# Kernel tuning notes

Hardware: AMD Instinct MI355X
Metric: run time of the kernel (lower is better)

Reference implementation:

```python
import jax, jax.numpy as jnp
import numpy as np
import math

D_MODEL = 1024
NUM_HEADS = 16
D_HEAD = D_MODEL // NUM_HEADS
BATCH = 2
SEQ = 2048


def setup_inputs() -> dict:
    key = jax.random.key(0)
    ks = jax.random.split(key, 5)
    sigma = math.sqrt(2.0 / (D_MODEL + D_MODEL))
    x = jax.random.normal(ks[0], (BATCH, SEQ, D_MODEL), dtype=jnp.float32)
    WQ = jax.random.normal(ks[1], (D_MODEL, D_MODEL), dtype=jnp.float32) * sigma
    WK = jax.random.normal(ks[2], (D_MODEL, D_MODEL), dtype=jnp.float32) * sigma
    WV = jax.random.normal(ks[3], (D_MODEL, D_MODEL), dtype=jnp.float32) * sigma
    WO = jax.random.normal(ks[4], (D_MODEL, D_MODEL), dtype=jnp.float32) * sigma
    return {"x": x, "WQ": WQ, "WK": WK, "WV": WV, "WO": WO}


def _softmax_fp32(scores):
    # matches custom softmax: compute in fp32, cast back to input dtype
    dtype = scores.dtype
    s = scores.astype(jnp.float32)
    return jax.nn.softmax(s, axis=-1).astype(dtype)


def reference(x, WQ, WK, WV, WO):
    batch, seq_len, _ = x.shape
    def split_heads(t):
        return t.reshape(batch, seq_len, NUM_HEADS, D_HEAD).transpose(0, 2, 1, 3)
    Q = split_heads(x @ WQ.T)  # [b,h,s,d]
    K = split_heads(x @ WK.T)
    V = split_heads(x @ WV.T)
    scale = 1.0 / math.sqrt(D_HEAD)
    scores = jnp.einsum('bhqd,bhkd->bhqk', Q, K) * scale
    # precomputed additive causal mask: 0 on/below diag, -inf above
    causal = jnp.triu(jnp.full((seq_len, seq_len), -jnp.inf, dtype=scores.dtype), k=1)
    scores = scores + causal
    attn = _softmax_fp32(scores)
    out = jnp.einsum('bhqk,bhkd->bhqd', attn, V)  # [b,h,s,d]
    out = out.transpose(0, 2, 1, 3).reshape(batch, seq_len, D_MODEL)
    return out @ WO.T
```

## Files before the change

### kernel.cpp

```cpp
#include <hip/hip_runtime.h>
#include <hip/hip_bf16.h>
#include <math.h>

typedef unsigned int u32;
typedef unsigned short u16;
typedef __attribute__((ext_vector_type(4))) float f32x4;
typedef __attribute__((ext_vector_type(4))) short bf16x4;
typedef __attribute__((ext_vector_type(8))) short bf16x8;
typedef __attribute__((ext_vector_type(4))) unsigned short u16x4;

#define D_MODEL 1024
#define SEQ     2048
#define NH      16
#define DH      64
#define MTOT    4096

#define QK_SCALE (0.125f * 1.44269504088896340736f)

__device__ __forceinline__ u16 f2bf(float f) {
  union { float f; u32 u; } a; a.f = f;
  u32 r = a.u + 0x7fffu + ((a.u >> 16) & 1u);
  return (u16)(r >> 16);
}

__device__ __forceinline__ u32 cvtpk(float lo, float hi) {
  u32 r;
  asm("v_cvt_pk_bf16_f32 %0, %1, %2" : "=v"(r) : "v"(lo), "v"(hi));
  return r;
}

__device__ __forceinline__ void async_copy16(const void* g, void* l) {
  __builtin_amdgcn_global_load_lds(
      (const __attribute__((address_space(1))) u32*)g,
      (__attribute__((address_space(3))) u32*)l, 16, 0, 0);
}

__global__ __launch_bounds__(256) void k_convert(
    const float* __restrict__ x,  const float* __restrict__ wq,
    const float* __restrict__ wk, const float* __restrict__ wv,
    const float* __restrict__ wo,
    u16* __restrict__ xb,  u16* __restrict__ wqb, u16* __restrict__ wkb,
    u16* __restrict__ wvb, u16* __restrict__ wob) {
  const long NX = (long)MTOT * D_MODEL / 8;
  const long NW = (long)D_MODEL * D_MODEL / 8;
  long i = (long)blockIdx.x * 256 + threadIdx.x;
  const float* src; u16* dst;
  if (i < NX)               { src = x;  dst = xb;  }
  else if (i < NX + NW)     { src = wq; dst = wqb; i -= NX; }
  else if (i < NX + 2*NW)   { src = wk; dst = wkb; i -= NX + 2*NW - NW; }
  else if (i < NX + 3*NW)   { src = wv; dst = wvb; i -= NX + 2*NW; }
  else                      { src = wo; dst = wob; i -= NX + 3*NW; }
  const f32x4* s4 = (const f32x4*)src + i * 2;
  f32x4 a = s4[0], b = s4[1];
  union { bf16x8 v; u16 e[8]; } o;
  o.e[0] = f2bf(a[0]); o.e[1] = f2bf(a[1]); o.e[2] = f2bf(a[2]); o.e[3] = f2bf(a[3]);
  o.e[4] = f2bf(b[0]); o.e[5] = f2bf(b[1]); o.e[6] = f2bf(b[2]); o.e[7] = f2bf(b[3]);
  *(bf16x8*)(dst + i * 8) = o.v;
}

__device__ __forceinline__ void gemm_core(
    const u16* __restrict__ A, const u16* __restrict__ Bm,
    u16* As, u16* Bs, f32x4 acc[4][4], int m0, int n0) {
  const int t = threadIdx.x;
  const int lane = t & 63, w = t >> 6;
  const int wr = (w >> 1) * 64, wc = (w & 1) * 64;
  const int lr = lane & 15, g = lane >> 4;
  const int rr = t >> 2, c8 = (t & 3) * 8;
#pragma unroll
  for (int mi = 0; mi < 4; ++mi)
#pragma unroll
    for (int ni = 0; ni < 4; ++ni)
      acc[mi][ni] = (f32x4){0.f, 0.f, 0.f, 0.f};
  const u16* ga0 = A  + (size_t)(m0 + rr) * D_MODEL + c8;
  const u16* ga1 = A  + (size_t)(m0 + 64 + rr) * D_MODEL + c8;
  const u16* gb0 = Bm + (size_t)(n0 + rr) * D_MODEL + c8;
  const u16* gb1 = Bm + (size_t)(n0 + 64 + rr) * D_MODEL + c8;
  async_copy16(ga0, As + t * 8);
  async_copy16(ga1, As + 2048 + t * 8);
  async_copy16(gb0, Bs + t * 8);
  async_copy16(gb1, Bs + 2048 + t * 8);
  int cur = 0;
  for (int k0 = 0; k0 < D_MODEL; k0 += 32) {
    __syncthreads();
    if (k0 + 32 < D_MODEL) {
      u16* Ad = As + (cur ^ 1) * 4096;
      u16* Bd = Bs + (cur ^ 1) * 4096;
      async_copy16(ga0 + k0 + 32, Ad + t * 8);
      async_copy16(ga1 + k0 + 32, Ad + 2048 + t * 8);
      async_copy16(gb0 + k0 + 32, Bd + t * 8);
      async_copy16(gb1 + k0 + 32, Bd + 2048 + t * 8);
    }
    const u16* Ab = As + cur * 4096;
    const u16* Bb = Bs + cur * 4096;
    bf16x8 af[4], bfr[4];
#pragma unroll
    for (int mi = 0; mi < 4; ++mi)
      af[mi] = *(const bf16x8*)(Ab + (wr + mi * 16 + lr) * 32 + g * 8);
#pragma unroll
    for (int ni = 0; ni < 4; ++ni)
      bfr[ni] = *(const bf16x8*)(Bb + (wc + ni * 16 + lr) * 32 + g * 8);
#pragma unroll
    for (int mi = 0; mi < 4; ++mi)
#pragma unroll
      for (int ni = 0; ni < 4; ++ni)
        acc[mi][ni] = __builtin_amdgcn_mfma_f32_16x16x32_bf16(
            af[mi], bfr[ni], acc[mi][ni], 0, 0, 0);
    cur ^= 1;
  }
}

__global__ __launch_bounds__(256) void k_gemm_qkv(
    const u16* __restrict__ xb, const u16* __restrict__ wqb,
    const u16* __restrict__ wkb, const u16* __restrict__ wvb,
    u16* __restrict__ Qo, u16* __restrict__ Ko, u16* __restrict__ Vt) {
  __shared__ u16 As[2 * 4096], Bs[2 * 4096];
  const int m0 = blockIdx.x * 128;
  const int n0g = blockIdx.y * 128;
  const int proj = n0g >> 10;
  const int n0 = n0g & 1023;
  const u16* Bm = (proj == 0) ? wqb : (proj == 1) ? wkb : wvb;
  const float scale = (proj == 0) ? QK_SCALE : 1.0f;
  f32x4 acc[4][4];
  gemm_core(xb, Bm, As, Bs, acc, m0, n0);
  const int t = threadIdx.x, lane = t & 63, w = t >> 6;
  const int wr = (w >> 1) * 64, wc = (w & 1) * 64;
  const int lr = lane & 15, g = lane >> 4;
  if (proj != 2) {
    u16* Out = (proj == 0) ? Qo : Ko;
#pragma unroll
    for (int mi = 0; mi < 4; ++mi)
#pragma unroll
      for (int ni = 0; ni < 4; ++ni)
#pragma unroll
        for (int jj = 0; jj < 4; ++jj) {
          int m = m0 + wr + mi * 16 + 4 * g + jj;
          int cn = n0 + wc + ni * 16 + lr;
          int h = cn >> 6, d = cn & 63;
          int b = m >> 11, s = m & 2047;
          Out[(((size_t)(b * NH + h) * SEQ) + s) * DH + d] =
              f2bf(acc[mi][ni][jj] * scale);
        }
  } else {
#pragma unroll
    for (int mi = 0; mi < 4; ++mi)
#pragma unroll
      for (int ni = 0; ni < 4; ++ni) {
        u16x4 pk;
#pragma unroll
        for (int jj = 0; jj < 4; ++jj) pk[jj] = f2bf(acc[mi][ni][jj]);
        int mb = m0 + wr + mi * 16 + 4 * g;
        int cn = n0 + wc + ni * 16 + lr;
        int h = cn >> 6, d = cn & 63;
        int b = mb >> 11, s = mb & 2047;
        *(u16x4*)(Vt + (((size_t)(b * NH + h) * DH + d) * SEQ) + s) = pk;
      }
  }
}

__global__ __launch_bounds__(256, 4) void k_attn(
    const u16* __restrict__ Q, const u16* __restrict__ K,
    const u16* __restrict__ Vt, u16* __restrict__ att) {
  __shared__ u16 Ksh[2][4096];
  __shared__ u16 Vsh[2][4096];
  const int t = threadIdx.x, lane = t & 63, w = t >> 6;
  const int lr = lane & 15, g = lane >> 4;
  const int bid = blockIdx.x;
  const int k4 = bid & 7;
  const int bh = (bid >> 3) & 31;
  const int j4 = bid >> 8;
  const int qb = (j4 == 0) ? (31 - k4) : (j4 == 1) ? k4
               : (j4 == 2) ? (23 - k4) : (8 + k4);
  const int q0 = qb * 64, qw = q0 + w * 16;
  const size_t hb = (size_t)bh * SEQ * DH;
  const u16* Qp  = Q  + hb;
  const u16* Kp  = K  + hb;
  const u16* Vtp = Vt + hb;

  bf16x8 qfr[2];
#pragma unroll
  for (int kk = 0; kk < 2; ++kk)
    qfr[kk] = *(const bf16x8*)(Qp + (size_t)(qw + lr) * DH + kk * 32 + g * 8);

  f32x4 o[4];
#pragma unroll
  for (int d = 0; d < 4; ++d) o[d] = (f32x4){0.f, 0.f, 0.f, 0.f};
  f32x4 lacc = (f32x4){0.f, 0.f, 0.f, 0.f};
  float mrow = -__builtin_inff();

  const short one_bf = (short)0x3F80;
  const bf16x8 onesb = {one_bf, one_bf, one_bf, one_bf,
                        one_bf, one_bf, one_bf, one_bf};

  const int sswz = ((t & 7) * 16) ^ (((t >> 3) & 7) << 4);
  const char* srcK = (const char*)Kp + (t >> 3) * 128 + sswz;
  const char* srcV = (const char*)Vtp + (t >> 3) * 4096 + sswz;

  const int nkv = qb + 1;
  int cur = 0;

  async_copy16(srcK,          (char*)&Ksh[0][0] + t * 16);
  async_copy16(srcK + 4096,   (char*)&Ksh[0][0] + 4096 + t * 16);
  async_copy16(srcV,          (char*)&Vsh[0][0] + t * 16);
  async_copy16(srcV + 131072, (char*)&Vsh[0][0] + 4096 + t * 16);

  for (int it = 0; it < nkv; ++it) {
    const int kv0 = it * 64;
    __syncthreads();
    if (it + 1 < nkv) {
      const char* sk = srcK + (size_t)(it + 1) * 8192;
      const char* sv = srcV + (size_t)(it + 1) * 128;
      char* kd = (char*)&Ksh[cur ^ 1][0];
      char* vd = (char*)&Vsh[cur ^ 1][0];
      async_copy16(sk,          kd + t * 16);
      async_copy16(sk + 4096,   kd + 4096 + t * 16);
      async_copy16(sv,          vd + t * 16);
      async_copy16(sv + 131072, vd + 4096 + t * 16);
    }
    if (kv0 <= qw + 15) {
      const char* kbase = (const char*)&Ksh[cur][0];
      const char* vbase = (const char*)&Vsh[cur][0];
      bf16x8 kfr[4][2];
#pragma unroll
      for (int mf = 0; mf < 4; ++mf) {
        int row = mf * 16 + lr;
#pragma unroll
        for (int kk = 0; kk < 2; ++kk) {
          int off = (row * 128 + kk * 64 + g * 16) ^ ((row & 7) << 4);
          kfr[mf][kk] = *(const bf16x8*)(kbase + off);
        }
      }
      f32x4 st[4];
#pragma unroll
      for (int mf = 0; mf < 4; ++mf) {
        f32x4 z = (f32x4){0.f, 0.f, 0.f, 0.f};
        z = __builtin_amdgcn_mfma_f32_16x16x32_bf16(kfr[mf][0], qfr[0], z, 0, 0, 0);
        st[mf] = __builtin_amdgcn_mfma_f32_16x16x32_bf16(kfr[mf][1], qfr[1], z, 0, 0, 0);
      }
      if (kv0 + 63 > qw) {
#pragma unroll
        for (int mf = 0; mf < 4; ++mf)
#pragma unroll
          for (int jj = 0; jj < 4; ++jj) {
            int kv = kv0 + mf * 16 + 4 * g + jj;
            st[mf][jj] = (kv > qw + lr) ? -__builtin_inff() : st[mf][jj];
          }
      }
      float v01 = fmaxf(fmaxf(fmaxf(st[0][0], st[0][1]), fmaxf(st[0][2], st[0][3])),
                        fmaxf(fmaxf(st[1][0], st[1][1]), fmaxf(st[1][2], st[1][3])));
      float v23 = fmaxf(fmaxf(fmaxf(st[2][0], st[2][1]), fmaxf(st[2][2], st[2][3])),
                        fmaxf(fmaxf(st[3][0], st[3][1]), fmaxf(st[3][2], st[3][3])));
      float v = fmaxf(v01, v23);
      v = fmaxf(v, __shfl_xor(v, 16));
      v = fmaxf(v, __shfl_xor(v, 32));
      if (__any(v > mrow + 8.0f)) {
        float mnew = fmaxf(mrow, v);
        float fac = exp2f(mrow - mnew);
        mrow = mnew;
        float fq[4];
#pragma unroll
        for (int jj = 0; jj < 4; ++jj)
          fq[jj] = __shfl(fac, 4 * g + jj);
#pragma unroll
        for (int d = 0; d < 4; ++d)
#pragma unroll
          for (int jj = 0; jj < 4; ++jj)
            o[d][jj] *= fq[jj];
#pragma unroll
        for (int jj = 0; jj < 4; ++jj)
          lacc[jj] *= fq[jj];
      }
      float p[4][4];
#pragma unroll
      for (int mf = 0; mf < 4; ++mf)
#pragma unroll
        for (int jj = 0; jj < 4; ++jj)
          p[mf][jj] = exp2f(st[mf][jj] - mrow);
      bf16x8 pa[2];
#pragma unroll
      for (int ks = 0; ks < 2; ++ks) {
        union { bf16x8 v8; u32 wdz[4]; } pu;
        pu.wdz[0] = cvtpk(p[ks * 2][0],     p[ks * 2][1]);
        pu.wdz[1] = cvtpk(p[ks * 2][2],     p[ks * 2][3]);
        pu.wdz[2] = cvtpk(p[ks * 2 + 1][0], p[ks * 2 + 1][1]);
        pu.wdz[3] = cvtpk(p[ks * 2 + 1][2], p[ks * 2 + 1][3]);
        pa[ks] = pu.v8;
      }
      lacc = __builtin_amdgcn_mfma_f32_16x16x32_bf16(pa[0], onesb, lacc, 0, 0, 0);
      lacc = __builtin_amdgcn_mfma_f32_16x16x32_bf16(pa[1], onesb, lacc, 0, 0, 0);
#pragma unroll
      for (int ks = 0; ks < 2; ++ks) {
        bf16x8 vb[4];
#pragma unroll
        for (int dd = 0; dd < 4; ++dd) {
          int row = dd * 16 + lr;
          int sz = (row & 7) << 4;
          union { bf16x8 v8; bf16x4 h[2]; } u;
          u.h[0] = *(const bf16x4*)(vbase + ((row * 128 + ks * 64 + g * 8) ^ sz));
          u.h[1] = *(const bf16x4*)(vbase + ((row * 128 + ks * 64 + 32 + g * 8) ^ sz));
          vb[dd] = u.v8;
        }
#pragma unroll
        for (int dd = 0; dd < 4; ++dd)
          o[dd] = __builtin_amdgcn_mfma_f32_16x16x32_bf16(pa[ks], vb[dd], o[dd], 0, 0, 0);
      }
    }
    cur ^= 1;
  }
  const int b = bh >> 4, h = bh & 15;
#pragma unroll
  for (int jj = 0; jj < 4; ++jj) {
    float li = 1.0f / lacc[jj];
    int q = qw + 4 * g + jj;
#pragma unroll
    for (int d = 0; d < 4; ++d) {
      int cn = h * 64 + d * 16 + lr;
      att[(size_t)(b * SEQ + q) * D_MODEL + cn] = f2bf(o[d][jj] * li);
    }
  }
}

__global__ __launch_bounds__(256) void k_gemm_out(
    const u16* __restrict__ att, const u16* __restrict__ wob,
    float* __restrict__ out) {
  __shared__ u16 As[2 * 4096], Bs[2 * 4096];
  const int m0 = blockIdx.x * 128, n0 = blockIdx.y * 128;
  f32x4 acc[4][4];
  gemm_core(att, wob, As, Bs, acc, m0, n0);
  const int t = threadIdx.x, lane = t & 63, w = t >> 6;
  const int wr = (w >> 1) * 64, wc = (w & 1) * 64;
  const int lr = lane & 15, g = lane >> 4;
#pragma unroll
  for (int mi = 0; mi < 4; ++mi)
#pragma unroll
    for (int ni = 0; ni < 4; ++ni)
#pragma unroll
      for (int jj = 0; jj < 4; ++jj) {
        int m = m0 + wr + mi * 16 + 4 * g + jj;
        int n = n0 + wc + ni * 16 + lr;
        out[(size_t)m * D_MODEL + n] = acc[mi][ni][jj];
      }
}

extern "C" void kernel_launch(void* const* d_in, const int* in_sizes, int n_in,
                              void* d_out, int out_size, void* d_ws, size_t ws_size,
                              hipStream_t stream) {
  (void)in_sizes; (void)n_in; (void)out_size; (void)ws_size;
  const float* x  = (const float*)d_in[0];
  const float* WQ = (const float*)d_in[1];
  const float* WK = (const float*)d_in[2];
  const float* WV = (const float*)d_in[3];
  const float* WO = (const float*)d_in[4];
  float* out = (float*)d_out;
  char* ws = (char*)d_ws;
  u16* xb  = (u16*)(ws);
  u16* wqb = (u16*)(ws + ((size_t)8 << 20));
  u16* wkb = (u16*)(ws + ((size_t)10 << 20));
  u16* wvb = (u16*)(ws + ((size_t)12 << 20));
  u16* wob = (u16*)(ws + ((size_t)14 << 20));
  u16* Qb  = (u16*)(ws + ((size_t)16 << 20));
  u16* Kb  = (u16*)(ws + ((size_t)24 << 20));
  u16* Vtb = (u16*)(ws + ((size_t)32 << 20));
  u16* att = (u16*)(ws + ((size_t)40 << 20));

  hipLaunchKernelGGL(k_convert, dim3(4096), dim3(256), 0, stream,
                     x, WQ, WK, WV, WO, xb, wqb, wkb, wvb, wob);
  hipLaunchKernelGGL(k_gemm_qkv, dim3(32, 24), dim3(256), 0, stream,
                     xb, wqb, wkb, wvb, Qb, Kb, Vtb);
  hipLaunchKernelGGL(k_attn, dim3(1024), dim3(256), 0, stream,
                     Qb, Kb, Vtb, att);
  hipLaunchKernelGGL(k_gemm_out, dim3(32, 8), dim3(256), 0, stream,
                     att, wob, out);
}
```

Measured before the change: 181.9 us.

## Use hardware exp2 and max3 in attention; retile output GEMM to 64x64

In the attention kernel, softmax exponentials now use the raw v_exp_f32 instruction instead of exp2f, and the row max is computed with three-input max operations. The output projection GEMM moves from 128x128 tiles over 256 blocks to its own 64x64-tile double-buffered loop over 1024 blocks, with a launch bound that allows more blocks per CU. This is meant to fill more CUs for the small output GEMM and to shorten the softmax instruction path. The smaller tiles give less data reuse per block, and the raw exp instruction skips exp2f's handling of denormal inputs.

```diff
diff --git a/kernel.cpp b/kernel.cpp
--- a/kernel.cpp
+++ b/kernel.cpp
@@ -27,6 +27,16 @@
   u32 r;
   asm("v_cvt_pk_bf16_f32 %0, %1, %2" : "=v"(r) : "v"(lo), "v"(hi));
   return r;
+}
+
+__device__ __forceinline__ float exp2_hw(float x) {
+  float r;
+  asm("v_exp_f32 %0, %1" : "=v"(r) : "v"(x));
+  return r;
+}
+
+__device__ __forceinline__ float fmax3(float a, float b, float c) {
+  return fmaxf(fmaxf(a, b), c);
 }
 
 __device__ __forceinline__ void async_copy16(const void* g, void* l) {
@@ -245,16 +255,18 @@
             st[mf][jj] = (kv > qw + lr) ? -__builtin_inff() : st[mf][jj];
           }
       }
-      float v01 = fmaxf(fmaxf(fmaxf(st[0][0], st[0][1]), fmaxf(st[0][2], st[0][3])),
-                        fmaxf(fmaxf(st[1][0], st[1][1]), fmaxf(st[1][2], st[1][3])));
-      float v23 = fmaxf(fmaxf(fmaxf(st[2][0], st[2][1]), fmaxf(st[2][2], st[2][3])),
-                        fmaxf(fmaxf(st[3][0], st[3][1]), fmaxf(st[3][2], st[3][3])));
-      float v = fmaxf(v01, v23);
+      float r1 = fmax3(st[0][0], st[0][1], st[0][2]);
+      float r2 = fmax3(st[0][3], st[1][0], st[1][1]);
+      float r3 = fmax3(st[1][2], st[1][3], st[2][0]);
+      float r4 = fmax3(st[2][1], st[2][2], st[2][3]);
+      float r5 = fmax3(st[3][0], st[3][1], st[3][2]);
+      float v = fmax3(fmax3(r1, r2, r3), fmax3(r4, r5, st[3][3]),
+                      -__builtin_inff());
       v = fmaxf(v, __shfl_xor(v, 16));
       v = fmaxf(v, __shfl_xor(v, 32));
       if (__any(v > mrow + 8.0f)) {
         float mnew = fmaxf(mrow, v);
-        float fac = exp2f(mrow - mnew);
+        float fac = exp2_hw(mrow - mnew);
         mrow = mnew;
         float fq[4];
 #pragma unroll
@@ -274,7 +286,7 @@
       for (int mf = 0; mf < 4; ++mf)
 #pragma unroll
         for (int jj = 0; jj < 4; ++jj)
-          p[mf][jj] = exp2f(st[mf][jj] - mrow);
+          p[mf][jj] = exp2_hw(st[mf][jj] - mrow);
       bf16x8 pa[2];
 #pragma unroll
       for (int ks = 0; ks < 2; ++ks) {
@@ -319,20 +331,53 @@
   }
 }
 
-__global__ __launch_bounds__(256) void k_gemm_out(
+__global__ __launch_bounds__(256, 4) void k_gemm_out(
     const u16* __restrict__ att, const u16* __restrict__ wob,
     float* __restrict__ out) {
-  __shared__ u16 As[2 * 4096], Bs[2 * 4096];
-  const int m0 = blockIdx.x * 128, n0 = blockIdx.y * 128;
-  f32x4 acc[4][4];
-  gemm_core(att, wob, As, Bs, acc, m0, n0);
+  __shared__ u16 As[2 * 2048], Bs[2 * 2048];
+  const int m0 = blockIdx.x * 64, n0 = blockIdx.y * 64;
   const int t = threadIdx.x, lane = t & 63, w = t >> 6;
-  const int wr = (w >> 1) * 64, wc = (w & 1) * 64;
+  const int wr = (w >> 1) * 32, wc = (w & 1) * 32;
   const int lr = lane & 15, g = lane >> 4;
-#pragma unroll
-  for (int mi = 0; mi < 4; ++mi)
-#pragma unroll
-    for (int ni = 0; ni < 4; ++ni)
+  const int rr = t >> 2, c8 = (t & 3) * 8;
+  f32x4 acc[2][2];
+#pragma unroll
+  for (int mi = 0; mi < 2; ++mi)
+#pragma unroll
+    for (int ni = 0; ni < 2; ++ni)
+      acc[mi][ni] = (f32x4){0.f, 0.f, 0.f, 0.f};
+  const u16* ga0 = att + (size_t)(m0 + rr) * D_MODEL + c8;
+  const u16* gb0 = wob + (size_t)(n0 + rr) * D_MODEL + c8;
+  async_copy16(ga0, As + t * 8);
+  async_copy16(gb0, Bs + t * 8);
+  int cur = 0;
+  for (int k0 = 0; k0 < D_MODEL; k0 += 32) {
+    __syncthreads();
+    if (k0 + 32 < D_MODEL) {
+      async_copy16(ga0 + k0 + 32, As + (cur ^ 1) * 2048 + t * 8);
+      async_copy16(gb0 + k0 + 32, Bs + (cur ^ 1) * 2048 + t * 8);
+    }
+    const u16* Ab = As + cur * 2048;
+    const u16* Bb = Bs + cur * 2048;
+    bf16x8 af[2], bfr[2];
+#pragma unroll
+    for (int mi = 0; mi < 2; ++mi)
+      af[mi] = *(const bf16x8*)(Ab + (wr + mi * 16 + lr) * 32 + g * 8);
+#pragma unroll
+    for (int ni = 0; ni < 2; ++ni)
+      bfr[ni] = *(const bf16x8*)(Bb + (wc + ni * 16 + lr) * 32 + g * 8);
+#pragma unroll
+    for (int mi = 0; mi < 2; ++mi)
+#pragma unroll
+      for (int ni = 0; ni < 2; ++ni)
+        acc[mi][ni] = __builtin_amdgcn_mfma_f32_16x16x32_bf16(
+            af[mi], bfr[ni], acc[mi][ni], 0, 0, 0);
+    cur ^= 1;
+  }
+#pragma unroll
+  for (int mi = 0; mi < 2; ++mi)
+#pragma unroll
+    for (int ni = 0; ni < 2; ++ni)
 #pragma unroll
       for (int jj = 0; jj < 4; ++jj) {
         int m = m0 + wr + mi * 16 + 4 * g + jj;
@@ -368,6 +413,6 @@
                      xb, wqb, wkb, wvb, Qb, Kb, Vtb);
   hipLaunchKernelGGL(k_attn, dim3(1024), dim3(256), 0, stream,
                      Qb, Kb, Vtb, att);
-  hipLaunchKernelGGL(k_gemm_out, dim3(32, 8), dim3(256), 0, stream,
+  hipLaunchKernelGGL(k_gemm_out, dim3(64, 16), dim3(256), 0, stream,
                      att, wob, out);
 }
```

Result: faster. 177.2 us (-2.6%).
